# Kernel tuning notes

Measured on AMD Instinct MI355X. Metric: run time of the kernel, lower is better.

Reference implementation:

```python
import jax, jax.numpy as jnp
import numpy as np

N, E, Z, H = 16384, 131072, 128, 8
ZH = Z // H
CUTOFF = 5.0


def _dense(key, din, dout, bias=True):
    kw, kb = jax.random.split(key)
    W = (jax.random.normal(kw, (din, dout), jnp.float32) / np.sqrt(din)).astype(jnp.float32)
    if bias:
        return W, jnp.zeros((dout,), jnp.float32)
    return W


def setup_inputs() -> dict:
    key = jax.random.key(0)
    ks = jax.random.split(key, 24)
    edge_index = jax.random.randint(ks[0], (2, E), 0, N)
    h_N_1_Z = jax.random.normal(ks[1], (N, 1, Z), jnp.float32)
    mu_N_L2_Z = jax.random.normal(ks[2], (N, 3, Z), jnp.float32) * 0.1
    ev = jax.random.normal(ks[3], (E, 3), jnp.float32)
    edge_vec_E_3 = ev / jnp.linalg.norm(ev, axis=-1, keepdims=True)
    edge_emb_E_Z = jax.random.normal(ks[4], (E, Z), jnp.float32)
    edge_weight_E = jax.random.uniform(ks[5], (E,), jnp.float32, 0.5, CUTOFF)
    deg = jax.ops.segment_sum(jnp.ones((E,), jnp.float32), edge_index[1], num_segments=N)
    num_edges_expanded_E = deg[edge_index[1]]
    inp = dict(edge_index=edge_index, h_N_1_Z=h_N_1_Z, mu_N_L2_Z=mu_N_L2_Z,
               edge_vec_E_3=edge_vec_E_3, edge_emb_E_Z=edge_emb_E_Z,
               edge_weight_E=edge_weight_E, num_edges_expanded_E=num_edges_expanded_E)
    inp['W_q'], inp['b_q'] = _dense(ks[6], Z, Z)
    inp['W_k'], inp['b_k'] = _dense(ks[7], Z, Z)
    inp['W_gs1'], inp['b_gs1'] = _dense(ks[8], Z, Z)
    inp['W_gs2'], inp['b_gs2'] = _dense(ks[9], Z, 3 * Z)
    inp['W_gv1'], inp['b_gv1'] = _dense(ks[10], Z, Z)
    inp['W_gv2'], inp['b_gv2'] = _dense(ks[11], Z, 3 * Z)
    inp['W_phik'], inp['b_phik'] = _dense(ks[12], Z, Z)
    inp['W_re'], inp['b_re'] = _dense(ks[13], Z, 3 * Z)
    inp['W_vq'] = _dense(ks[14], Z, Z, bias=False)   # vecq_w, no bias
    inp['W_vk0'] = _dense(ks[15], Z, Z, bias=False)  # veck_w[0] (lmax=1), no bias
    inp['W_lin'], inp['b_lin'] = _dense(ks[16], Z, Z)  # lin_w_linear
    inp['W_eu1'], inp['b_eu1'] = _dense(ks[17], Z, Z)  # edge_attr_up MLP [Z,Z,Z]
    inp['W_eu2'], inp['b_eu2'] = _dense(ks[18], Z, Z)
    return inp


def reference(edge_index, h_N_1_Z, mu_N_L2_Z, edge_vec_E_3, edge_emb_E_Z,
              edge_weight_E, num_edges_expanded_E,
              W_q, b_q, W_k, b_k, W_gs1, b_gs1, W_gs2, b_gs2,
              W_gv1, b_gv1, W_gv2, b_gv2, W_phik, b_phik, W_re, b_re,
              W_vq, W_vk0, W_lin, b_lin, W_eu1, b_eu1, W_eu2, b_eu2):
    silu = jax.nn.silu
    src, dst = edge_index[0], edge_index[1]  # messages j->i aggregated at dst=i
    hs = h_N_1_Z[:, 0]                        # (N, Z); layernorm='' -> identity
    q = (hs @ W_q + b_q).reshape(N, H, ZH)
    k = (hs @ W_k + b_k).reshape(N, H, ZH)
    x3 = silu(hs @ W_gs1 + b_gs1) @ W_gs2 + b_gs2    # gamma_s: (N, 3Z)
    val3 = silu(hs @ W_gv1 + b_gv1) @ W_gv2 + b_gv2  # gamma_v: (N, 3Z)
    r_attn = silu(edge_emb_E_Z @ W_phik + b_phik).reshape(E, H, ZH)
    r_ij = edge_emb_E_Z @ W_re + b_re                # (E, 3Z)

    # per-edge multi-head attention with segment softmax over target node
    logits = jnp.sum(q[dst] * k[src] * r_attn, axis=-1)        # (E, H)
    m = jax.ops.segment_max(logits, dst, num_segments=N)
    ex = jnp.exp(logits - m[dst])
    den = jax.ops.segment_sum(ex, dst, num_segments=N)
    attn = ex / den[dst]
    attn = attn * (jnp.sqrt(num_edges_expanded_E)[:, None] / np.float32(np.sqrt(Z)))

    sea = (attn[..., None] * val3[src].reshape(E, H, 3 * ZH)).reshape(E, 3 * Z)
    cut = 0.5 * (jnp.cos(jnp.pi * edge_weight_E / CUTOFF) + 1.0) * (edge_weight_E < CUTOFF)
    x_ij = cut[:, None] * sea * (x3[src] * r_ij)               # (E, 3Z)
    o_s, o_d, o_t = x_ij[:, :Z], x_ij[:, Z:2 * Z], x_ij[:, 2 * Z:]
    dmu_ij = o_d[:, None, :] * edge_vec_E_3[..., None] + o_t[:, None, :] * mu_N_L2_Z[src]  # (E,3,Z)

    h_out = h_N_1_Z + jax.ops.segment_sum(o_s, dst, num_segments=N)[:, None, :]
    mu_out = mu_N_L2_Z + jax.ops.segment_sum(dmu_ij, dst, num_segments=N)

    # edge update (sep_vecj, lmax=1 -> single degree block)
    w1 = jnp.einsum('nlz,ze->nle', mu_out, W_vq)
    w2 = jnp.einsum('nlz,ze->nle', mu_out, W_vk0)
    w1_d = jnp.sum(w1[dst] * edge_vec_E_3[..., None], axis=1)  # (E, evec)
    w2_d = jnp.sum(w2[src] * edge_vec_E_3[..., None], axis=1)
    w_dot = jnp.tanh((w1_d * w2_d) @ W_lin + b_lin)            # gated='gatedt'
    f_up = silu(edge_emb_E_Z @ W_eu1 + b_eu1) @ W_eu2 + b_eu2  # edge_attr_up MLP
    df_ij = edge_emb_E_Z + f_up * w_dot
    return h_out, mu_out, df_ij
```

## Files before the change

### kernel.cpp

```cpp
#include <hip/hip_runtime.h>
#include <math.h>

#define NN 16384
#define EE 131072
#define ZZ 128
#define HH 8

typedef short bf16x8 __attribute__((ext_vector_type(8)));
typedef float f32x4 __attribute__((ext_vector_type(4)));
typedef unsigned short ushort4v __attribute__((ext_vector_type(4)));
typedef unsigned short ushort8v __attribute__((ext_vector_type(8)));

__device__ __forceinline__ float silu_f(float x) { return x / (1.0f + __expf(-x)); }

__device__ __forceinline__ unsigned short f2bf(float x) {
    unsigned u = __float_as_uint(x);
    unsigned r = (u >> 16) & 1u;
    u += 0x7fffu + r;
    return (unsigned short)(u >> 16);
}
__device__ __forceinline__ float bf2f(unsigned short x) {
    return __uint_as_float(((unsigned)x) << 16);
}

__device__ __forceinline__ f32x4 mfma16(bf16x8 a, bf16x8 b, f32x4 c) {
    return __builtin_amdgcn_mfma_f32_16x16x32_bf16(a, b, c, 0, 0, 0);
}

__device__ __forceinline__ void stageB(const unsigned short* Wt, char* lB, int t) {
    const uint4* Wg = (const uint4*)Wt;
#pragma unroll
    for (int i = 0; i < 8; ++i) {
        const int cid = t + i * 256;
        const int n = cid >> 4, c16 = cid & 15;
        *(uint4*)(lB + ((n * 256 + c16 * 16) ^ ((n & 7) << 4))) = Wg[cid];
    }
}

struct WPrep {
    const float* w[13];
    int P[13];
    int tile0[14];
};

__global__ __launch_bounds__(128) void prep_weights(WPrep wp, unsigned short* wt) {
    int b = blockIdx.x, wi = 0;
    while (b >= wp.tile0[wi + 1]) ++wi;
    const int cg = (b - wp.tile0[wi]) * 128;
    const float* w = wp.w[wi];
    unsigned short* o = wt + (size_t)wp.tile0[wi] * 16384;
    const int P = wp.P[wi];
    const int t = threadIdx.x;
    for (int k0 = 0; k0 < 128; k0 += 8) {
        ushort8v v;
#pragma unroll
        for (int j = 0; j < 8; ++j) v[j] = f2bf(w[(size_t)(k0 + j) * P + cg + t]);
        *(ushort8v*)(o + (size_t)(cg + t) * 128 + k0) = v;
    }
}

struct BPrep {
    const float* b[13];
    int off[14];
};

__global__ __launch_bounds__(256) void prep_bias(BPrep bp, float* bcat) {
    const int idx = blockIdx.x * 256 + threadIdx.x;
    if (idx >= 2432) return;
    int wi = 0;
    while (idx >= bp.off[wi + 1]) ++wi;
    bcat[idx] = bp.b[wi] ? bp.b[wi][idx - bp.off[wi]] : 0.f;
}

__global__ __launch_bounds__(256) void prep_mub(const float* __restrict__ mu,
                                                unsigned short* __restrict__ mub) {
    const size_t idx = (size_t)blockIdx.x * 256 + threadIdx.x;
    const float4 a = ((const float4*)mu)[idx * 2];
    const float4 b = ((const float4*)mu)[idx * 2 + 1];
    ushort8v v;
    v[0] = f2bf(a.x); v[1] = f2bf(a.y); v[2] = f2bf(a.z); v[3] = f2bf(a.w);
    v[4] = f2bf(b.x); v[5] = f2bf(b.y); v[6] = f2bf(b.z); v[7] = f2bf(b.w);
    *(ushort8v*)(mub + idx * 8) = v;
}

template <int ACT, int INBF, int DUMP>
__global__ __launch_bounds__(256, 2) void mm_bf16(
    const void* __restrict__ Av, const unsigned short* __restrict__ Wt,
    const float* __restrict__ bias, unsigned short* __restrict__ C,
    const unsigned short* __restrict__ aux, unsigned short* __restrict__ dumpA,
    int P, int As)
{
    __shared__ uint4 lA4[2048];
    __shared__ uint4 lB4[2048];
    char* lA = (char*)lA4;
    char* lB = (char*)lB4;
    const int t = threadIdx.x;
    const size_t row0 = (size_t)blockIdx.x * 128;
    const int cg = blockIdx.y * 128;
    if (INBF) {
        const uint4* Ag = (const uint4*)((const unsigned short*)Av + row0 * As);
        const int rs = As >> 3;
#pragma unroll
        for (int i = 0; i < 8; ++i) {
            const int chunk = t + i * 256;
            const int r = chunk >> 4, c16 = chunk & 15;
            *(uint4*)(lA + ((r * 256 + c16 * 16) ^ ((r & 7) << 4))) = Ag[r * rs + c16];
        }
    } else {
        const float4* Ag = (const float4*)((const float*)Av + row0 * As);
        const int rs = As >> 2;
#pragma unroll
        for (int i = 0; i < 16; ++i) {
            const int f4 = t + i * 256;
            const int r = f4 >> 5, c4 = f4 & 31;
            const float4 v = Ag[r * rs + c4];
            ushort4v bb;
            bb.x = f2bf(v.x); bb.y = f2bf(v.y); bb.z = f2bf(v.z); bb.w = f2bf(v.w);
            *(ushort4v*)(lA + ((r * 256 + c4 * 8) ^ ((r & 7) << 4))) = bb;
        }
    }
    stageB(Wt + (size_t)cg * 128, lB, t);
    __syncthreads();
    if (DUMP) {
#pragma unroll
        for (int i = 0; i < 8; ++i) {
            const int ch = t + i * 256;
            const int row = ch >> 4, cpos = ch & 15;
            const uint4 v = *(const uint4*)(lA + ((row * 256 + cpos * 16) ^ ((row & 7) << 4)));
            *(uint4*)(dumpA + (row0 + row) * 128 + cpos * 8) = v;
        }
    }
    const int lane = t & 63, wid = t >> 6;
    const int rbase = (wid >> 1) * 64, cbase = (wid & 1) * 64;
    const int lr = lane & 15, lgp = lane >> 4;
    f32x4 acc[4][4];
#pragma unroll
    for (int i = 0; i < 4; ++i)
#pragma unroll
        for (int j = 0; j < 4; ++j) acc[i][j] = (f32x4){0.f, 0.f, 0.f, 0.f};
#pragma unroll
    for (int ks = 0; ks < 4; ++ks) {
        bf16x8 av[4], bv[4];
#pragma unroll
        for (int mt = 0; mt < 4; ++mt) {
            const int r = rbase + mt * 16 + lr;
            av[mt] = *(const bf16x8*)(lA + ((r * 256 + ks * 64 + lgp * 16) ^ ((r & 7) << 4)));
        }
#pragma unroll
        for (int nt = 0; nt < 4; ++nt) {
            const int c = cbase + nt * 16 + lr;
            bv[nt] = *(const bf16x8*)(lB + ((c * 256 + ks * 64 + lgp * 16) ^ ((c & 7) << 4)));
        }
#pragma unroll
        for (int mt = 0; mt < 4; ++mt)
#pragma unroll
            for (int nt = 0; nt < 4; ++nt)
                acc[mt][nt] = mfma16(av[mt], bv[nt], acc[mt][nt]);
    }
    __syncthreads();
#pragma unroll
    for (int nt = 0; nt < 4; ++nt) {
        const int col = cbase + nt * 16 + lr;
        const int gcol = cg + col;
        const float b = bias[gcol];
#pragma unroll
        for (int mt = 0; mt < 4; ++mt) {
#pragma unroll
            for (int j = 0; j < 4; ++j) {
                const int row = rbase + mt * 16 + lgp * 4 + j;
                float v = acc[mt][nt][j] + b;
                if (ACT == 1) v = silu_f(v);
                if (ACT == 2) v = v * bf2f(aux[(row0 + row) * (size_t)P + gcol]);
                *(unsigned short*)(lB + ((row * 256 + col * 2) ^ ((row & 7) << 4))) = f2bf(v);
            }
        }
    }
    __syncthreads();
#pragma unroll
    for (int i = 0; i < 8; ++i) {
        const int ch = t + i * 256;
        const int row = ch >> 4, cpos = ch & 15;
        const uint4 v = *(const uint4*)(lB + ((row * 256 + cpos * 16) ^ ((row & 7) << 4)));
        *(uint4*)(C + (row0 + row) * (size_t)P + cg + cpos * 8) = v;
    }
}

__global__ __launch_bounds__(256) void attn_kernel(
    const int* __restrict__ row_start, const int* __restrict__ perm,
    const int* __restrict__ srcp, const unsigned short* __restrict__ qkb,
    const unsigned short* __restrict__ rab, const float* __restrict__ ewp,
    float* __restrict__ attnw)
{
    const int t = threadIdx.x;
    const int n = blockIdx.x * 4 + (t >> 6);
    const int lane = t & 63;
    const int el = lane >> 3, h = lane & 7;
    const int beg = row_start[n], end = row_start[n + 1];
    if (beg == end) return;
    const ushort8v q0 = *(const ushort8v*)(qkb + (size_t)n * 256 + h * 16);
    const ushort8v q1 = *(const ushort8v*)(qkb + (size_t)n * 256 + h * 16 + 8);
    float m = -1e30f, den = 0.f;
    for (int i0 = beg; i0 < end; i0 += 8) {
        const int i = i0 + el;
        const bool valid = i < end;
        const int ii = valid ? i : beg;
        const int e = perm[ii];
        const int s = srcp[ii];
        const ushort8v k0 = *(const ushort8v*)(qkb + (size_t)s * 256 + 128 + h * 16);
        const ushort8v k1 = *(const ushort8v*)(qkb + (size_t)s * 256 + 128 + h * 16 + 8);
        const ushort8v r0 = *(const ushort8v*)(rab + (size_t)e * 128 + h * 16);
        const ushort8v r1 = *(const ushort8v*)(rab + (size_t)e * 128 + h * 16 + 8);
        float lgv = 0.f;
#pragma unroll
        for (int j = 0; j < 8; ++j) lgv += bf2f(q0[j]) * bf2f(k0[j]) * bf2f(r0[j]);
#pragma unroll
        for (int j = 0; j < 8; ++j) lgv += bf2f(q1[j]) * bf2f(k1[j]) * bf2f(r1[j]);
        if (!valid) lgv = -1e30f;
        else attnw[(size_t)i * 8 + h] = lgv;
        float cm = lgv;
        cm = fmaxf(cm, __shfl_xor(cm, 8));
        cm = fmaxf(cm, __shfl_xor(cm, 16));
        cm = fmaxf(cm, __shfl_xor(cm, 32));
        const float nm = fmaxf(m, cm);
        float ex = valid ? __expf(lgv - nm) : 0.f;
        float cd = ex;
        cd += __shfl_xor(cd, 8);
        cd += __shfl_xor(cd, 16);
        cd += __shfl_xor(cd, 32);
        den = den * __expf(m - nm) + cd;
        m = nm;
    }
    const float sc = sqrtf((float)(end - beg)) * 0.08838834764831845f / den;
    for (int i0 = beg; i0 < end; i0 += 8) {
        const int i = i0 + el;
        if (i >= end) continue;
        const float w = ewp[i];
        const float cut = (w < 5.0f) ? 0.5f * (cosf(w * 0.62831853071795864f) + 1.0f) : 0.0f;
        const float lgv = attnw[(size_t)i * 8 + h];
        attnw[(size_t)i * 8 + h] = __expf(lgv - m) * sc * cut;
    }
}

__global__ __launch_bounds__(256, 4) void combine_mfma(
    const unsigned short* __restrict__ embb, const int* __restrict__ perm,
    const unsigned short* __restrict__ Wt_re, const float* __restrict__ bre,
    const float* __restrict__ attnw, unsigned short* __restrict__ ob)
{
    __shared__ uint4 lA4[2048];
    __shared__ float attnS[128 * 8];
    __shared__ int permS[128];
    char* lA = (char*)lA4;
    const int t = threadIdx.x;
    const size_t e0 = (size_t)blockIdx.x * 128;
    if (t < 128) permS[t] = perm[e0 + t];
    ((float4*)attnS)[t] = ((const float4*)(attnw + e0 * 8))[t];
    __syncthreads();
#pragma unroll
    for (int i = 0; i < 8; ++i) {
        const int chunk = t + i * 256;
        const int r = chunk >> 4, c16 = chunk & 15;
        const uint4 v = *(const uint4*)(embb + (size_t)permS[r] * 128 + c16 * 8);
        *(uint4*)(lA + ((r * 256 + c16 * 16) ^ ((r & 7) << 4))) = v;
    }
    __syncthreads();
    const int lane = t & 63, wid = t >> 6;
    const int rbase = (wid >> 1) * 64, cbase = (wid & 1) * 64;
    const int lr = lane & 15, lgp = lane >> 4;
    for (int cg3 = 0; cg3 < 3; ++cg3) {
        const unsigned short* Wp = Wt_re + (size_t)cg3 * 16384;
        f32x4 acc[4][4];
#pragma unroll
        for (int i = 0; i < 4; ++i)
#pragma unroll
            for (int j = 0; j < 4; ++j) acc[i][j] = (f32x4){0.f, 0.f, 0.f, 0.f};
#pragma unroll
        for (int ks = 0; ks < 4; ++ks) {
            bf16x8 av[4], bv[4];
#pragma unroll
            for (int mt = 0; mt < 4; ++mt) {
                const int r = rbase + mt * 16 + lr;
                av[mt] = *(const bf16x8*)(lA + ((r * 256 + ks * 64 + lgp * 16) ^ ((r & 7) << 4)));
            }
#pragma unroll
            for (int nt = 0; nt < 4; ++nt)
                bv[nt] = *(const bf16x8*)(Wp + (size_t)(cbase + nt * 16 + lr) * 128 + ks * 32 + lgp * 8);
#pragma unroll
            for (int mt = 0; mt < 4; ++mt)
#pragma unroll
                for (int nt = 0; nt < 4; ++nt)
                    acc[mt][nt] = mfma16(bv[nt], av[mt], acc[mt][nt]);
        }
        const int cgo = cg3 * 128;
#pragma unroll
        for (int mt = 0; mt < 4; ++mt) {
            const int row = rbase + mt * 16 + lr;
            const float* aS = attnS + row * 8;
#pragma unroll
            for (int nt = 0; nt < 4; ++nt) {
                const int col0 = cbase + nt * 16 + lgp * 4;
                const int gcol = cgo + col0;
                const float coef = aS[gcol / 48];
                const float4 b4 = *(const float4*)(bre + gcol);
                ushort4v st;
                st.x = f2bf((acc[mt][nt][0] + b4.x) * coef);
                st.y = f2bf((acc[mt][nt][1] + b4.y) * coef);
                st.z = f2bf((acc[mt][nt][2] + b4.z) * coef);
                st.w = f2bf((acc[mt][nt][3] + b4.w) * coef);
                *(ushort4v*)(ob + (e0 + row) * 384 + gcol) = st;
            }
        }
    }
}

__global__ __launch_bounds__(256, 3) void wdot_fused(
    const unsigned short* __restrict__ w12, const float* __restrict__ ev,
    const int* __restrict__ src, const int* __restrict__ dst,
    const unsigned short* __restrict__ Wt_lin, const float* __restrict__ bl,
    const unsigned short* __restrict__ embb, const unsigned short* __restrict__ fup,
    float* __restrict__ df)
{
    __shared__ uint4 lA4[2048];
    char* lA = (char*)lA4;
    const int t = threadIdx.x;
    const size_t e0 = (size_t)blockIdx.x * 128;
#pragma unroll
    for (int i = 0; i < 8; ++i) {
        const int chunk = t + i * 256;
        const int r = chunk >> 4, c8 = chunk & 15;
        const size_t e = e0 + r;
        const int s = src[e], d = dst[e];
        const float e0v = ev[e * 3 + 0], e1v = ev[e * 3 + 1], e2v = ev[e * 3 + 2];
        const ushort8v a0 = *(const ushort8v*)(w12 + ((size_t)d * 3 + 0) * 256 + c8 * 8);
        const ushort8v a1 = *(const ushort8v*)(w12 + ((size_t)d * 3 + 1) * 256 + c8 * 8);
        const ushort8v a2 = *(const ushort8v*)(w12 + ((size_t)d * 3 + 2) * 256 + c8 * 8);
        const ushort8v c0 = *(const ushort8v*)(w12 + ((size_t)s * 3 + 0) * 256 + 128 + c8 * 8);
        const ushort8v c1 = *(const ushort8v*)(w12 + ((size_t)s * 3 + 1) * 256 + 128 + c8 * 8);
        const ushort8v c2 = *(const ushort8v*)(w12 + ((size_t)s * 3 + 2) * 256 + 128 + c8 * 8);
        ushort8v o;
#pragma unroll
        for (int j = 0; j < 8; ++j) {
            const float av = e0v * bf2f(a0[j]) + e1v * bf2f(a1[j]) + e2v * bf2f(a2[j]);
            const float bv = e0v * bf2f(c0[j]) + e1v * bf2f(c1[j]) + e2v * bf2f(c2[j]);
            o[j] = f2bf(av * bv);
        }
        *(ushort8v*)(lA + ((r * 256 + c8 * 16) ^ ((r & 7) << 4))) = o;
    }
    __syncthreads();
    const int lane = t & 63, wid = t >> 6;
    const int rbase = (wid >> 1) * 64, cbase = (wid & 1) * 64;
    const int lr = lane & 15, lgp = lane >> 4;
    f32x4 acc[4][4];
#pragma unroll
    for (int i = 0; i < 4; ++i)
#pragma unroll
        for (int j = 0; j < 4; ++j) acc[i][j] = (f32x4){0.f, 0.f, 0.f, 0.f};
#pragma unroll
    for (int ks = 0; ks < 4; ++ks) {
        bf16x8 av[4], bv[4];
#pragma unroll
        for (int mt = 0; mt < 4; ++mt) {
            const int r = rbase + mt * 16 + lr;
            av[mt] = *(const bf16x8*)(lA + ((r * 256 + ks * 64 + lgp * 16) ^ ((r & 7) << 4)));
        }
#pragma unroll
        for (int nt = 0; nt < 4; ++nt)
            bv[nt] = *(const bf16x8*)(Wt_lin + (size_t)(cbase + nt * 16 + lr) * 128 + ks * 32 + lgp * 8);
#pragma unroll
        for (int mt = 0; mt < 4; ++mt)
#pragma unroll
            for (int nt = 0; nt < 4; ++nt)
                acc[mt][nt] = mfma16(bv[nt], av[mt], acc[mt][nt]);
    }
#pragma unroll
    for (int mt = 0; mt < 4; ++mt) {
        const int row = rbase + mt * 16 + lr;
#pragma unroll
        for (int nt = 0; nt < 4; ++nt) {
            const int col0 = cbase + nt * 16 + lgp * 4;
            const float4 b4 = *(const float4*)(bl + col0);
            const size_t base = (e0 + row) * 128 + col0;
            const ushort4v em = *(const ushort4v*)(embb + base);
            const ushort4v fu = *(const ushort4v*)(fup + base);
            float4 o;
            o.x = bf2f(em.x) + bf2f(fu.x) * tanhf(acc[mt][nt][0] + b4.x);
            o.y = bf2f(em.y) + bf2f(fu.y) * tanhf(acc[mt][nt][1] + b4.y);
            o.z = bf2f(em.z) + bf2f(fu.z) * tanhf(acc[mt][nt][2] + b4.z);
            o.w = bf2f(em.w) + bf2f(fu.w) * tanhf(acc[mt][nt][3] + b4.w);
            *(float4*)(df + base) = o;
        }
    }
}

__global__ __launch_bounds__(256) void hist_kernel(const int* __restrict__ dst, int* __restrict__ counts) {
    const int e = blockIdx.x * 256 + threadIdx.x;
    atomicAdd(&counts[dst[e]], 1);
}

__global__ __launch_bounds__(256) void scan_kernel(const int* __restrict__ counts,
                                                   int* __restrict__ row_start,
                                                   int* __restrict__ cursor) {
    __shared__ int part[256];
    const int t = threadIdx.x;
    const int base = t * 64;
    int local[64];
    int s = 0;
#pragma unroll
    for (int i = 0; i < 64; ++i) { local[i] = s; s += counts[base + i]; }
    part[t] = s;
    __syncthreads();
    for (int off = 1; off < 256; off <<= 1) {
        int v = (t >= off) ? part[t - off] : 0;
        __syncthreads();
        part[t] += v;
        __syncthreads();
    }
    const int prev = (t == 0) ? 0 : part[t - 1];
#pragma unroll
    for (int i = 0; i < 64; ++i) {
        const int v = prev + local[i];
        row_start[base + i] = v;
        cursor[base + i] = v;
    }
    if (t == 255) row_start[NN] = prev + s;
}

__global__ __launch_bounds__(256) void fill_kernel(
    const int* __restrict__ src, const int* __restrict__ dst,
    const float* __restrict__ ewt, const float* __restrict__ ev,
    int* __restrict__ cursor, int* __restrict__ perm,
    int* __restrict__ srcp, float* __restrict__ ewp, float* __restrict__ evp)
{
    const int e = blockIdx.x * 256 + threadIdx.x;
    const int p = atomicAdd(&cursor[dst[e]], 1);
    perm[p] = e;
    srcp[p] = src[e];
    ewp[p] = ewt[e];
    evp[p * 3 + 0] = ev[e * 3 + 0];
    evp[p * 3 + 1] = ev[e * 3 + 1];
    evp[p * 3 + 2] = ev[e * 3 + 2];
}

__global__ __launch_bounds__(256) void gather_kernel(
    const int* __restrict__ row_start, const int* __restrict__ srcp,
    const unsigned short* __restrict__ ob, const unsigned short* __restrict__ xv,
    const unsigned short* __restrict__ mub, const float* __restrict__ evp,
    const float* __restrict__ h_in, const float* __restrict__ mu_in,
    float* __restrict__ h_out, float* __restrict__ mu_out)
{
    const int n = blockIdx.x * 2 + (threadIdx.x >> 7);
    const int t = threadIdx.x & 127;
    const int beg = row_start[n], end = row_start[n + 1];
    float hacc = h_in[(size_t)n * 128 + t];
    float m0 = mu_in[(size_t)n * 384 + t];
    float m1 = mu_in[(size_t)n * 384 + 128 + t];
    float m2 = mu_in[(size_t)n * 384 + 256 + t];
    for (int i = beg; i < end; ++i) {
        const int s = srcp[i];
        const float e0 = evp[i * 3 + 0], e1 = evp[i * 3 + 1], e2 = evp[i * 3 + 2];
        const unsigned short* op = ob + (size_t)i * 384 + t;
        const unsigned short* xp = xv + (size_t)s * 384 + t;
        const unsigned short* mp = mub + (size_t)s * 384 + t;
        const float osv = bf2f(op[0]) * bf2f(xp[0]);
        const float odv = bf2f(op[128]) * bf2f(xp[128]);
        const float otv = bf2f(op[256]) * bf2f(xp[256]);
        hacc += osv;
        m0 += odv * e0 + otv * bf2f(mp[0]);
        m1 += odv * e1 + otv * bf2f(mp[128]);
        m2 += odv * e2 + otv * bf2f(mp[256]);
    }
    h_out[(size_t)n * 128 + t] = hacc;
    mu_out[(size_t)n * 384 + t] = m0;
    mu_out[(size_t)n * 384 + 128 + t] = m1;
    mu_out[(size_t)n * 384 + 256 + t] = m2;
}

extern "C" void kernel_launch(void* const* d_in, const int* in_sizes, int n_in,
                              void* d_out, int out_size, void* d_ws, size_t ws_size,
                              hipStream_t stream) {
    const int* eidx = (const int*)d_in[0];
    const int* src = eidx;
    const int* dst = eidx + EE;
    const float* h_in  = (const float*)d_in[1];
    const float* mu_in = (const float*)d_in[2];
    const float* ev    = (const float*)d_in[3];
    const float* emb   = (const float*)d_in[4];
    const float* ewt   = (const float*)d_in[5];
    const float* W_q   = (const float*)d_in[7];  const float* b_q   = (const float*)d_in[8];
    const float* W_k   = (const float*)d_in[9];  const float* b_k   = (const float*)d_in[10];
    const float* W_gs1 = (const float*)d_in[11]; const float* b_gs1 = (const float*)d_in[12];
    const float* W_gs2 = (const float*)d_in[13]; const float* b_gs2 = (const float*)d_in[14];
    const float* W_gv1 = (const float*)d_in[15]; const float* b_gv1 = (const float*)d_in[16];
    const float* W_gv2 = (const float*)d_in[17]; const float* b_gv2 = (const float*)d_in[18];
    const float* W_phik= (const float*)d_in[19]; const float* b_phik= (const float*)d_in[20];
    const float* W_re  = (const float*)d_in[21]; const float* b_re  = (const float*)d_in[22];
    const float* W_vq  = (const float*)d_in[23];
    const float* W_vk0 = (const float*)d_in[24];
    const float* W_lin = (const float*)d_in[25]; const float* b_lin = (const float*)d_in[26];
    const float* W_eu1 = (const float*)d_in[27]; const float* b_eu1 = (const float*)d_in[28];
    const float* W_eu2 = (const float*)d_in[29]; const float* b_eu2 = (const float*)d_in[30];

    float* out    = (float*)d_out;
    float* h_out  = out;
    float* mu_out = out + (size_t)NN * ZZ;
    float* df     = out + (size_t)NN * ZZ * 4;

    const size_t NZ = (size_t)NN * ZZ, N3Z = (size_t)NN * 3 * ZZ, EZ = (size_t)EE * ZZ;
    const size_t EH = (size_t)EE * HH;
    char* p = (char*)d_ws;
    unsigned short* qkb   = (unsigned short*)p; p += NZ * 2 * 2;
    unsigned short* tmpn2 = (unsigned short*)p; p += NZ * 2 * 2;
    unsigned short* x3b   = (unsigned short*)p; p += N3Z * 2;
    unsigned short* xv    = (unsigned short*)p; p += N3Z * 2;
    unsigned short* mub   = (unsigned short*)p; p += N3Z * 2;
    unsigned short* w12   = (unsigned short*)p; p += N3Z * 2 * 2;
    unsigned short* embb  = (unsigned short*)p; p += EZ * 2;
    unsigned short* rab   = (unsigned short*)p; p += EZ * 2;
    unsigned short* tmpe  = (unsigned short*)p; p += EZ * 2;
    unsigned short* fup   = (unsigned short*)p; p += EZ * 2;
    unsigned short* ob    = (unsigned short*)p; p += EZ * 3 * 2;
    float* attnw          = (float*)p;          p += EH * 4;
    unsigned short* wt    = (unsigned short*)p; p += 2432 * 128 * 2;
    float* bcat           = (float*)p;          p += 2432 * 4;
    int* counts           = (int*)p;            p += NN * 4;
    int* cursor           = (int*)p;            p += NN * 4;
    int* row_start        = (int*)p;            p += (NN + 1) * 4;
    int* perm             = (int*)p;            p += EE * 4;
    int* srcp             = (int*)p;            p += EE * 4;
    float* ewp            = (float*)p;          p += EE * 4;
    float* evp            = (float*)p;          p += EE * 12;

    const float* wsrc[13] = {W_q, W_k, W_gs1, W_gv1, W_gs2, W_gv2, W_phik,
                             W_re, W_vq, W_vk0, W_lin, W_eu1, W_eu2};
    const float* bsrc[13] = {b_q, b_k, b_gs1, b_gv1, b_gs2, b_gv2, b_phik,
                             b_re, nullptr, nullptr, b_lin, b_eu1, b_eu2};
    const int Ps[13] = {128, 128, 128, 128, 384, 384, 128, 384, 128, 128, 128, 128, 128};
    WPrep wp; BPrep bp;
    int tiles = 0;
    for (int i = 0; i < 13; ++i) {
        wp.w[i] = wsrc[i]; wp.P[i] = Ps[i]; wp.tile0[i] = tiles;
        bp.b[i] = bsrc[i]; bp.off[i] = tiles * 128;
        tiles += Ps[i] / 128;
    }
    wp.tile0[13] = tiles; bp.off[13] = tiles * 128;
    unsigned short* wT[13]; const float* bC[13];
    for (int i = 0; i < 13; ++i) { wT[i] = wt + (size_t)wp.tile0[i] * 16384; bC[i] = bcat + bp.off[i]; }

    dim3 blk(256);
    prep_weights<<<dim3(tiles), dim3(128), 0, stream>>>(wp, wt);
    prep_bias<<<dim3(10), blk, 0, stream>>>(bp, bcat);
    prep_mub<<<dim3(N3Z / 8 / 256), blk, 0, stream>>>(mu_in, mub);
    mm_bf16<0,0,0><<<dim3(NN/128, 2), blk, 0, stream>>>(h_in, wT[0], bC[0], qkb, nullptr, nullptr, 256, 128);
    mm_bf16<1,0,0><<<dim3(NN/128, 2), blk, 0, stream>>>(h_in, wT[2], bC[2], tmpn2, nullptr, nullptr, 256, 128);
    mm_bf16<0,1,0><<<dim3(NN/128, 3), blk, 0, stream>>>(tmpn2, wT[4], bC[4], x3b, nullptr, nullptr, 384, 256);
    mm_bf16<2,1,0><<<dim3(NN/128, 3), blk, 0, stream>>>(tmpn2 + 128, wT[5], bC[5], xv, x3b, nullptr, 384, 256);
    mm_bf16<1,0,1><<<dim3(EE/128, 1), blk, 0, stream>>>(emb, wT[11], bC[11], tmpe, nullptr, embb, 128, 128);
    mm_bf16<0,1,0><<<dim3(EE/128, 1), blk, 0, stream>>>(tmpe, wT[12], bC[12], fup, nullptr, nullptr, 128, 128);
    mm_bf16<1,1,0><<<dim3(EE/128, 1), blk, 0, stream>>>(embb, wT[6], bC[6], rab, nullptr, nullptr, 128, 128);
    hipMemsetAsync(counts, 0, NN * 4, stream);
    hist_kernel<<<dim3(EE/256), blk, 0, stream>>>(dst, counts);
    scan_kernel<<<dim3(1), blk, 0, stream>>>(counts, row_start, cursor);
    fill_kernel<<<dim3(EE/256), blk, 0, stream>>>(src, dst, ewt, ev, cursor, perm, srcp, ewp, evp);
    attn_kernel<<<dim3(NN/4), blk, 0, stream>>>(row_start, perm, srcp, qkb, rab, ewp, attnw);
    combine_mfma<<<dim3(EE/128), blk, 0, stream>>>(embb, perm, wT[7], bC[7], attnw, ob);
    gather_kernel<<<dim3(NN/2), blk, 0, stream>>>(
        row_start, srcp, ob, xv, mub, evp, h_in, mu_in, h_out, mu_out);
    mm_bf16<0,0,0><<<dim3(3*NN/128, 2), blk, 0, stream>>>(mu_out, wT[8], bC[8], w12, nullptr, nullptr, 256, 128);
    wdot_fused<<<dim3(EE/128), blk, 0, stream>>>(
        w12, ev, src, dst, wT[10], bC[10], embb, fup, df);
}
```

Baseline: 438.1 us.

## Scatter edge matmul outputs into dst-sorted order to avoid perm gathers

Fill now records each edge's sorted position (inverse permutation), and the phi_k matmul scatters its output and a copy of the bf16 edge embedding into dst-sorted rows. Attention and combine then read rab and emb contiguously instead of gathering through perm. Combine also keeps its A fragments in registers and stages outputs through LDS so the global stores are coalesced 16-byte writes. The cost is an extra sorted embedding buffer, scattered row writes, and higher register pressure in combine.

```diff
diff --git a/kernel.cpp b/kernel.cpp
--- a/kernel.cpp
+++ b/kernel.cpp
@@ -83,12 +83,12 @@
     *(ushort8v*)(mub + idx * 8) = v;
 }
 
-template <int ACT, int INBF, int DUMP>
+template <int ACT, int INBF, int DUMP, int PERM>
 __global__ __launch_bounds__(256, 2) void mm_bf16(
     const void* __restrict__ Av, const unsigned short* __restrict__ Wt,
     const float* __restrict__ bias, unsigned short* __restrict__ C,
     const unsigned short* __restrict__ aux, unsigned short* __restrict__ dumpA,
-    int P, int As)
+    const int* __restrict__ rowmap, int P, int As)
 {
     __shared__ uint4 lA4[2048];
     __shared__ uint4 lB4[2048];
@@ -127,7 +127,8 @@
             const int ch = t + i * 256;
             const int row = ch >> 4, cpos = ch & 15;
             const uint4 v = *(const uint4*)(lA + ((row * 256 + cpos * 16) ^ ((row & 7) << 4)));
-            *(uint4*)(dumpA + (row0 + row) * 128 + cpos * 8) = v;
+            const size_t orow = PERM ? (size_t)rowmap[row0 + row] : row0 + row;
+            *(uint4*)(dumpA + orow * 128 + cpos * 8) = v;
         }
     }
     const int lane = t & 63, wid = t >> 6;
@@ -181,15 +182,15 @@
         const int ch = t + i * 256;
         const int row = ch >> 4, cpos = ch & 15;
         const uint4 v = *(const uint4*)(lB + ((row * 256 + cpos * 16) ^ ((row & 7) << 4)));
-        *(uint4*)(C + (row0 + row) * (size_t)P + cg + cpos * 8) = v;
+        const size_t orow = PERM ? (size_t)rowmap[row0 + row] : row0 + row;
+        *(uint4*)(C + orow * (size_t)P + cg + cpos * 8) = v;
     }
 }
 
 __global__ __launch_bounds__(256) void attn_kernel(
-    const int* __restrict__ row_start, const int* __restrict__ perm,
-    const int* __restrict__ srcp, const unsigned short* __restrict__ qkb,
-    const unsigned short* __restrict__ rab, const float* __restrict__ ewp,
-    float* __restrict__ attnw)
+    const int* __restrict__ row_start, const int* __restrict__ srcp,
+    const unsigned short* __restrict__ qkb, const unsigned short* __restrict__ rabp,
+    const float* __restrict__ ewp, float* __restrict__ attnw)
 {
     const int t = threadIdx.x;
     const int n = blockIdx.x * 4 + (t >> 6);
@@ -204,12 +205,11 @@
         const int i = i0 + el;
         const bool valid = i < end;
         const int ii = valid ? i : beg;
-        const int e = perm[ii];
         const int s = srcp[ii];
         const ushort8v k0 = *(const ushort8v*)(qkb + (size_t)s * 256 + 128 + h * 16);
         const ushort8v k1 = *(const ushort8v*)(qkb + (size_t)s * 256 + 128 + h * 16 + 8);
-        const ushort8v r0 = *(const ushort8v*)(rab + (size_t)e * 128 + h * 16);
-        const ushort8v r1 = *(const ushort8v*)(rab + (size_t)e * 128 + h * 16 + 8);
+        const ushort8v r0 = *(const ushort8v*)(rabp + (size_t)ii * 128 + h * 16);
+        const ushort8v r1 = *(const ushort8v*)(rabp + (size_t)ii * 128 + h * 16 + 8);
         float lgv = 0.f;
 #pragma unroll
         for (int j = 0; j < 8; ++j) lgv += bf2f(q0[j]) * bf2f(k0[j]) * bf2f(r0[j]);
@@ -242,30 +242,38 @@
 }
 
 __global__ __launch_bounds__(256, 4) void combine_mfma(
-    const unsigned short* __restrict__ embb, const int* __restrict__ perm,
-    const unsigned short* __restrict__ Wt_re, const float* __restrict__ bre,
-    const float* __restrict__ attnw, unsigned short* __restrict__ ob)
+    const unsigned short* __restrict__ embp, const unsigned short* __restrict__ Wt_re,
+    const float* __restrict__ bre, const float* __restrict__ attnw,
+    unsigned short* __restrict__ ob)
 {
     __shared__ uint4 lA4[2048];
     __shared__ float attnS[128 * 8];
-    __shared__ int permS[128];
     char* lA = (char*)lA4;
     const int t = threadIdx.x;
     const size_t e0 = (size_t)blockIdx.x * 128;
-    if (t < 128) permS[t] = perm[e0 + t];
+    {
+        const uint4* Ag = (const uint4*)(embp + e0 * 128);
+#pragma unroll
+        for (int i = 0; i < 8; ++i) {
+            const int chunk = t + i * 256;
+            const int r = chunk >> 4, c16 = chunk & 15;
+            *(uint4*)(lA + ((r * 256 + c16 * 16) ^ ((r & 7) << 4))) = Ag[chunk];
+        }
+    }
     ((float4*)attnS)[t] = ((const float4*)(attnw + e0 * 8))[t];
-    __syncthreads();
-#pragma unroll
-    for (int i = 0; i < 8; ++i) {
-        const int chunk = t + i * 256;
-        const int r = chunk >> 4, c16 = chunk & 15;
-        const uint4 v = *(const uint4*)(embb + (size_t)permS[r] * 128 + c16 * 8);
-        *(uint4*)(lA + ((r * 256 + c16 * 16) ^ ((r & 7) << 4))) = v;
-    }
     __syncthreads();
     const int lane = t & 63, wid = t >> 6;
     const int rbase = (wid >> 1) * 64, cbase = (wid & 1) * 64;
     const int lr = lane & 15, lgp = lane >> 4;
+    bf16x8 avh[4][4];
+#pragma unroll
+    for (int ks = 0; ks < 4; ++ks)
+#pragma unroll
+        for (int mt = 0; mt < 4; ++mt) {
+            const int r = rbase + mt * 16 + lr;
+            avh[ks][mt] = *(const bf16x8*)(lA + ((r * 256 + ks * 64 + lgp * 16) ^ ((r & 7) << 4)));
+        }
+    __syncthreads();
     for (int cg3 = 0; cg3 < 3; ++cg3) {
         const unsigned short* Wp = Wt_re + (size_t)cg3 * 16384;
         f32x4 acc[4][4];
@@ -275,12 +283,7 @@
             for (int j = 0; j < 4; ++j) acc[i][j] = (f32x4){0.f, 0.f, 0.f, 0.f};
 #pragma unroll
         for (int ks = 0; ks < 4; ++ks) {
-            bf16x8 av[4], bv[4];
-#pragma unroll
-            for (int mt = 0; mt < 4; ++mt) {
-                const int r = rbase + mt * 16 + lr;
-                av[mt] = *(const bf16x8*)(lA + ((r * 256 + ks * 64 + lgp * 16) ^ ((r & 7) << 4)));
-            }
+            bf16x8 bv[4];
 #pragma unroll
             for (int nt = 0; nt < 4; ++nt)
                 bv[nt] = *(const bf16x8*)(Wp + (size_t)(cbase + nt * 16 + lr) * 128 + ks * 32 + lgp * 8);
@@ -288,7 +291,7 @@
             for (int mt = 0; mt < 4; ++mt)
 #pragma unroll
                 for (int nt = 0; nt < 4; ++nt)
-                    acc[mt][nt] = mfma16(bv[nt], av[mt], acc[mt][nt]);
+                    acc[mt][nt] = mfma16(bv[nt], avh[ks][mt], acc[mt][nt]);
         }
         const int cgo = cg3 * 128;
 #pragma unroll
@@ -306,9 +309,18 @@
                 st.y = f2bf((acc[mt][nt][1] + b4.y) * coef);
                 st.z = f2bf((acc[mt][nt][2] + b4.z) * coef);
                 st.w = f2bf((acc[mt][nt][3] + b4.w) * coef);
-                *(ushort4v*)(ob + (e0 + row) * 384 + gcol) = st;
+                *(ushort4v*)(lA + ((row * 256 + col0 * 2) ^ ((row & 7) << 4))) = st;
             }
         }
+        __syncthreads();
+#pragma unroll
+        for (int i = 0; i < 8; ++i) {
+            const int ch = t + i * 256;
+            const int row = ch >> 4, cpos = ch & 15;
+            const uint4 v = *(const uint4*)(lA + ((row * 256 + cpos * 16) ^ ((row & 7) << 4)));
+            *(uint4*)(ob + (e0 + row) * 384 + cgo + cpos * 8) = v;
+        }
+        __syncthreads();
     }
 }
 
@@ -427,12 +439,12 @@
 __global__ __launch_bounds__(256) void fill_kernel(
     const int* __restrict__ src, const int* __restrict__ dst,
     const float* __restrict__ ewt, const float* __restrict__ ev,
-    int* __restrict__ cursor, int* __restrict__ perm,
+    int* __restrict__ cursor, int* __restrict__ ip,
     int* __restrict__ srcp, float* __restrict__ ewp, float* __restrict__ evp)
 {
     const int e = blockIdx.x * 256 + threadIdx.x;
     const int p = atomicAdd(&cursor[dst[e]], 1);
-    perm[p] = e;
+    ip[e] = p;
     srcp[p] = src[e];
     ewp[p] = ewt[e];
     evp[p * 3 + 0] = ev[e * 3 + 0];
@@ -514,7 +526,8 @@
     unsigned short* mub   = (unsigned short*)p; p += N3Z * 2;
     unsigned short* w12   = (unsigned short*)p; p += N3Z * 2 * 2;
     unsigned short* embb  = (unsigned short*)p; p += EZ * 2;
-    unsigned short* rab   = (unsigned short*)p; p += EZ * 2;
+    unsigned short* embp  = (unsigned short*)p; p += EZ * 2;
+    unsigned short* rabp  = (unsigned short*)p; p += EZ * 2;
     unsigned short* tmpe  = (unsigned short*)p; p += EZ * 2;
     unsigned short* fup   = (unsigned short*)p; p += EZ * 2;
     unsigned short* ob    = (unsigned short*)p; p += EZ * 3 * 2;
@@ -524,7 +537,7 @@
     int* counts           = (int*)p;            p += NN * 4;
     int* cursor           = (int*)p;            p += NN * 4;
     int* row_start        = (int*)p;            p += (NN + 1) * 4;
-    int* perm             = (int*)p;            p += EE * 4;
+    int* ip               = (int*)p;            p += EE * 4;
     int* srcp             = (int*)p;            p += EE * 4;
     float* ewp            = (float*)p;          p += EE * 4;
     float* evp            = (float*)p;          p += EE * 12;
@@ -549,22 +562,22 @@
     prep_weights<<<dim3(tiles), dim3(128), 0, stream>>>(wp, wt);
     prep_bias<<<dim3(10), blk, 0, stream>>>(bp, bcat);
     prep_mub<<<dim3(N3Z / 8 / 256), blk, 0, stream>>>(mu_in, mub);
-    mm_bf16<0,0,0><<<dim3(NN/128, 2), blk, 0, stream>>>(h_in, wT[0], bC[0], qkb, nullptr, nullptr, 256, 128);
-    mm_bf16<1,0,0><<<dim3(NN/128, 2), blk, 0, stream>>>(h_in, wT[2], bC[2], tmpn2, nullptr, nullptr, 256, 128);
-    mm_bf16<0,1,0><<<dim3(NN/128, 3), blk, 0, stream>>>(tmpn2, wT[4], bC[4], x3b, nullptr, nullptr, 384, 256);
-    mm_bf16<2,1,0><<<dim3(NN/128, 3), blk, 0, stream>>>(tmpn2 + 128, wT[5], bC[5], xv, x3b, nullptr, 384, 256);
-    mm_bf16<1,0,1><<<dim3(EE/128, 1), blk, 0, stream>>>(emb, wT[11], bC[11], tmpe, nullptr, embb, 128, 128);
-    mm_bf16<0,1,0><<<dim3(EE/128, 1), blk, 0, stream>>>(tmpe, wT[12], bC[12], fup, nullptr, nullptr, 128, 128);
-    mm_bf16<1,1,0><<<dim3(EE/128, 1), blk, 0, stream>>>(embb, wT[6], bC[6], rab, nullptr, nullptr, 128, 128);
     hipMemsetAsync(counts, 0, NN * 4, stream);
     hist_kernel<<<dim3(EE/256), blk, 0, stream>>>(dst, counts);
     scan_kernel<<<dim3(1), blk, 0, stream>>>(counts, row_start, cursor);
-    fill_kernel<<<dim3(EE/256), blk, 0, stream>>>(src, dst, ewt, ev, cursor, perm, srcp, ewp, evp);
-    attn_kernel<<<dim3(NN/4), blk, 0, stream>>>(row_start, perm, srcp, qkb, rab, ewp, attnw);
-    combine_mfma<<<dim3(EE/128), blk, 0, stream>>>(embb, perm, wT[7], bC[7], attnw, ob);
+    fill_kernel<<<dim3(EE/256), blk, 0, stream>>>(src, dst, ewt, ev, cursor, ip, srcp, ewp, evp);
+    mm_bf16<0,0,0,0><<<dim3(NN/128, 2), blk, 0, stream>>>(h_in, wT[0], bC[0], qkb, nullptr, nullptr, nullptr, 256, 128);
+    mm_bf16<1,0,0,0><<<dim3(NN/128, 2), blk, 0, stream>>>(h_in, wT[2], bC[2], tmpn2, nullptr, nullptr, nullptr, 256, 128);
+    mm_bf16<0,1,0,0><<<dim3(NN/128, 3), blk, 0, stream>>>(tmpn2, wT[4], bC[4], x3b, nullptr, nullptr, nullptr, 384, 256);
+    mm_bf16<2,1,0,0><<<dim3(NN/128, 3), blk, 0, stream>>>(tmpn2 + 128, wT[5], bC[5], xv, x3b, nullptr, nullptr, 384, 256);
+    mm_bf16<1,0,1,0><<<dim3(EE/128, 1), blk, 0, stream>>>(emb, wT[11], bC[11], tmpe, nullptr, embb, nullptr, 128, 128);
+    mm_bf16<0,1,0,0><<<dim3(EE/128, 1), blk, 0, stream>>>(tmpe, wT[12], bC[12], fup, nullptr, nullptr, nullptr, 128, 128);
+    mm_bf16<1,1,1,1><<<dim3(EE/128, 1), blk, 0, stream>>>(embb, wT[6], bC[6], rabp, nullptr, embp, ip, 128, 128);
+    attn_kernel<<<dim3(NN/4), blk, 0, stream>>>(row_start, srcp, qkb, rabp, ewp, attnw);
+    combine_mfma<<<dim3(EE/128), blk, 0, stream>>>(embp, wT[7], bC[7], attnw, ob);
     gather_kernel<<<dim3(NN/2), blk, 0, stream>>>(
         row_start, srcp, ob, xv, mub, evp, h_in, mu_in, h_out, mu_out);
-    mm_bf16<0,0,0><<<dim3(3*NN/128, 2), blk, 0, stream>>>(mu_out, wT[8], bC[8], w12, nullptr, nullptr, 256, 128);
+    mm_bf16<0,0,0,0><<<dim3(3*NN/128, 2), blk, 0, stream>>>(mu_out, wT[8], bC[8], w12, nullptr, nullptr, nullptr, 256, 128);
     wdot_fused<<<dim3(EE/128), blk, 0, stream>>>(
         w12, ev, src, dst, wT[10], bC[10], embb, fup, df);
 }
```

After: 474.0 us. 8.2% more time.
